# Performance work log

Measured on AMD Instinct MI355X. Metric: run time of the kernel, lower is better.

The kernel has to match this reference:

```python
import jax, jax.numpy as jnp
import numpy as np

SEQ, BS, DIM = 2048, 2, 256
G, NQ = 2, 8           # n_keys groups, n_queries total
SUB = NQ // G          # queries per group
EPS = 1e-5


def _ln(x, gamma, beta):
    m = jnp.mean(x, axis=-1, keepdims=True)
    v = jnp.mean(jnp.square(x - m), axis=-1, keepdims=True)
    return (x - m) * jax.lax.rsqrt(v + EPS) * gamma + beta


def setup_inputs() -> dict:
    key = jax.random.key(0)
    ks = jax.random.split(key, 16)
    s = 0.02
    return {
        "x":   jax.random.normal(ks[0], (SEQ, BS, DIM), jnp.float32),
        # block layernorms
        "g0": jnp.ones((DIM,), jnp.float32), "b0": jnp.zeros((DIM,), jnp.float32),
        "g1": jnp.ones((DIM,), jnp.float32), "b1": jnp.zeros((DIM,), jnp.float32),
        # attention q/k layernorm (norm_kvs=True)
        "gn": jnp.ones((DIM,), jnp.float32), "bn": jnp.zeros((DIM,), jnp.float32),
        # attention projections (torch Linear: weight [out,in])
        "wk": jax.random.normal(ks[1], (DIM * G, DIM), jnp.float32) * s,
        "bk": jnp.zeros((DIM * G,), jnp.float32),
        "wv": jax.random.normal(ks[2], (DIM * G, DIM), jnp.float32) * s,
        "bv": jnp.zeros((DIM * G,), jnp.float32),
        "wq": jax.random.normal(ks[3], (DIM * NQ, DIM), jnp.float32) * s,
        "bq": jnp.zeros((DIM * NQ,), jnp.float32),
        "wo": jax.random.normal(ks[4], (DIM, DIM * NQ), jnp.float32) * s,
        "bo": jnp.zeros((DIM,), jnp.float32),
        # FFN: BayesLora(dim,2dim) -> relu -> BayesLora(2dim,dim), eval == plain linear
        "w1": jax.random.normal(ks[5], (2 * DIM, DIM), jnp.float32) * s,
        "bf1": jnp.zeros((2 * DIM,), jnp.float32),
        "w2": jax.random.normal(ks[6], (DIM, 2 * DIM), jnp.float32) * s,
        "bf2": jnp.zeros((DIM,), jnp.float32),
    }


def reference(x, g0, b0, g1, b1, gn, bn, wk, bk, wv, bv, wq, bq, wo, bo, w1, bf1, w2, bf2):
    seq, bs, dim = x.shape
    # --- attention (pre-norm) ---
    h = _ln(x, g0, b0)                                        # s b d
    K = (h @ wk.T + bk).reshape(seq, bs, G, dim)              # s b g i
    V = (h @ wv.T + bv).reshape(seq, bs, G, dim)              # s b g i
    Q = (h @ wq.T + bq).reshape(seq, bs, G, SUB, dim)         # s b g u i
    K = _ln(K, gn, bn)
    Q = _ln(Q, gn, bn)
    scores = jnp.einsum('sbgui,tbgi->bgust', Q, K) / jnp.sqrt(jnp.float32(dim))
    neg = jnp.finfo(scores.dtype).min
    causal = jnp.tril(jnp.ones((seq, seq), bool))             # s1 >= s2 allowed
    scores = jnp.where(causal, scores, neg)
    probs = jax.nn.softmax(scores, axis=-1)                   # b g u s t
    out = jnp.einsum('bgust,tbgi->sbgui', probs, V)
    out = out.reshape(seq, bs, G * SUB * dim)                 # s b (g u i)
    x = x + (out @ wo.T + bo)
    # --- FFN (pre-norm) ---
    h2 = _ln(x, g1, b1)
    f = jax.nn.relu(h2 @ w1.T + bf1) @ w2.T + bf2
    return x + f
```

## Files before the change

kernel.cpp:

```cpp
#include <hip/hip_runtime.h>
#include <hip/hip_bf16.h>

#define SEQ  2048
#define BSZ  2
#define DIM  256
#define NG   2
#define NQH  8
#define SUBQ 4
#define ROWS (SEQ*BSZ)
#define NQKV 3072
#define QROW 6144

typedef unsigned int uint32;
typedef unsigned short ushort;
typedef __attribute__((ext_vector_type(8))) short short8;
typedef __attribute__((ext_vector_type(4))) float f32x4;

__device__ __forceinline__ float bflo(uint32 u){
  union { uint32 i; float f; } c; c.i = u << 16; return c.f;
}
__device__ __forceinline__ float bfhi(uint32 u){
  union { uint32 i; float f; } c; c.i = u & 0xffff0000u; return c.f;
}
__device__ __forceinline__ uint32 pack2(float a, float b){
  __hip_bfloat16 ha = __float2bfloat16(a);
  __hip_bfloat16 hb = __float2bfloat16(b);
  unsigned short ua, ub;
  __builtin_memcpy(&ua, &ha, 2);
  __builtin_memcpy(&ub, &hb, 2);
  return (uint32)ua | ((uint32)ub << 16);
}
__device__ __forceinline__ ushort bf16bits(float v){
  __hip_bfloat16 h = __float2bfloat16(v);
  ushort u; __builtin_memcpy(&u, &h, 2); return u;
}

__device__ __forceinline__ void dma16(const void* g, void* l) {
  __builtin_amdgcn_global_load_lds(
      (const __attribute__((address_space(1))) uint32*)g,
      (__attribute__((address_space(3))) uint32*)l, 16, 0, 0);
}

__global__ __launch_bounds__(256) void wcvt6(
    const float* __restrict__ wk, const float* __restrict__ wv,
    const float* __restrict__ wq, const float* __restrict__ wo,
    const float* __restrict__ w1, const float* __restrict__ w2,
    const float* __restrict__ bk, const float* __restrict__ bv,
    const float* __restrict__ bq,
    __hip_bfloat16* __restrict__ out, float* __restrict__ bc)
{
  int e4 = blockIdx.x * 256 + threadIdx.x;
  if (e4 < 393216) {
    const float* src; int loc;
    if      (e4 <  32768) { src = wk; loc = e4; }
    else if (e4 <  65536) { src = wv; loc = e4 -  32768; }
    else if (e4 < 196608) { src = wq; loc = e4 -  65536; }
    else if (e4 < 327680) { src = wo; loc = e4 - 196608; }
    else if (e4 < 360448) { src = w1; loc = e4 - 327680; }
    else                  { src = w2; loc = e4 - 360448; }
    float4 v = *(const float4*)(src + 4 * (size_t)loc);
    uint2 st; st.x = pack2(v.x, v.y); st.y = pack2(v.z, v.w);
    *(uint2*)(out + 4 * (size_t)e4) = st;
  } else {
    int u = e4 - 393216;
    const float* src; int loc;
    if      (u < 128) { src = bk; loc = u; }
    else if (u < 256) { src = bv; loc = u - 128; }
    else              { src = bq; loc = u - 256; }
    *(float4*)(bc + 4 * (size_t)u) = *(const float4*)(src + 4 * (size_t)loc);
  }
}

__global__ __launch_bounds__(256) void ln_rows_w(
    const float* __restrict__ in,
    const float* __restrict__ gamma,
    const float* __restrict__ beta,
    __hip_bfloat16* __restrict__ out)
{
  int wave = threadIdx.x >> 6, lane = threadIdx.x & 63;
  int row = blockIdx.x * 4 + wave;
  size_t base = (size_t)row * DIM + lane * 4;
  float4 v = *(const float4*)(in + base);
  float s  = v.x + v.y + v.z + v.w;
  float s2 = v.x*v.x + v.y*v.y + v.z*v.z + v.w*v.w;
  #pragma unroll
  for (int o = 1; o < 64; o <<= 1) {
    s  += __shfl_xor(s, o);
    s2 += __shfl_xor(s2, o);
  }
  float m = s * (1.0f / DIM);
  float rb = rsqrtf(s2 * (1.0f / DIM) - m * m + 1e-5f);
  float4 gm = *(const float4*)(gamma + lane * 4);
  float4 bt = *(const float4*)(beta + lane * 4);
  uint2 st;
  st.x = pack2((v.x - m) * rb * gm.x + bt.x, (v.y - m) * rb * gm.y + bt.y);
  st.y = pack2((v.z - m) * rb * gm.z + bt.z, (v.w - m) * rb * gm.w + bt.w);
  *(uint2*)(out + base) = st;
}

__global__ __launch_bounds__(256) void ln_qkv_w(
    __hip_bfloat16* __restrict__ QKV,
    const float* __restrict__ gamma,
    const float* __restrict__ beta)
{
  int wave = threadIdx.x >> 6, lane = threadIdx.x & 63;
  int idx = blockIdx.x * 4 + wave;
  size_t base;
  if (idx < ROWS * NG) {
    base = (size_t)(idx >> 1) * NQKV + (idx & 1) * DIM;
  } else {
    int j = idx - ROWS * NG;
    base = (size_t)(j >> 3) * NQKV + 2 * NG * DIM + (j & 7) * DIM;
  }
  __hip_bfloat16* p = QKV + base + lane * 4;
  uint2 u = *(const uint2*)p;
  float v0 = bflo(u.x), v1 = bfhi(u.x), v2 = bflo(u.y), v3 = bfhi(u.y);
  float s  = v0 + v1 + v2 + v3;
  float s2 = v0*v0 + v1*v1 + v2*v2 + v3*v3;
  #pragma unroll
  for (int o = 1; o < 64; o <<= 1) {
    s  += __shfl_xor(s, o);
    s2 += __shfl_xor(s2, o);
  }
  float m = s * (1.0f / DIM);
  float rb = rsqrtf(s2 * (1.0f / DIM) - m * m + 1e-5f);
  float4 gm = *(const float4*)(gamma + lane * 4);
  float4 bt = *(const float4*)(beta + lane * 4);
  uint2 st;
  st.x = pack2((v0 - m) * rb * gm.x + bt.x, (v1 - m) * rb * gm.y + bt.y);
  st.y = pack2((v2 - m) * rb * gm.z + bt.z, (v3 - m) * rb * gm.w + bt.w);
  *(uint2*)p = st;
}

__global__ __launch_bounds__(256) void v_transpose(
    const __hip_bfloat16* __restrict__ QKV, __hip_bfloat16* __restrict__ VT)
{
  __shared__ ushort T[64][72];
  int t0 = blockIdx.x * 64, d0 = blockIdx.y * 64, bg = blockIdx.z;
  int b = bg >> 1, g = bg & 1;
  int tid = threadIdx.x;
  int tr = tid >> 2, c4 = (tid & 3) * 16;
  const ushort* src = (const ushort*)QKV + ((size_t)(t0 + tr) * BSZ + b) * NQKV
                    + NG * DIM + g * DIM + d0 + c4;
  uint4 a0 = *(const uint4*)src;
  uint4 a1 = *(const uint4*)(src + 8);
  *(uint4*)&T[tr][c4]     = a0;
  *(uint4*)&T[tr][c4 + 8] = a1;
  __syncthreads();
  ushort tmp[16];
  #pragma unroll
  for (int i = 0; i < 16; ++i) tmp[i] = T[c4 + i][tr];
  ushort* dst = (ushort*)VT + ((size_t)bg * DIM + d0 + tr) * SEQ + t0 + c4;
  *(uint4*)dst       = *(uint4*)&tmp[0];
  *(uint4*)(dst + 8) = *(uint4*)&tmp[8];
}

template<int GN, int RELU, int OUTMODE>
__global__ __launch_bounds__(256) void gemm_mfma(
    const __hip_bfloat16* __restrict__ A,
    const __hip_bfloat16* __restrict__ W,
    const float* __restrict__ bias,
    const float* __restrict__ resid,
    void* __restrict__ outp,
    int M, int N, int K)
{
  constexpr int WCH = GN / 16;
  constexpr int MC  = (GN == 128) ? 4 : 2;
  __shared__ __align__(16) ushort AS[2][4096];
  __shared__ __align__(16) ushort WS[2][WCH * 512];

  const int tid = threadIdx.x;
  const int wave = tid >> 6, lane = tid & 63;
  const int col = lane & 15, quad = lane >> 4;
  const int wm = (GN == 128) ? (wave >> 1) : wave;
  const int wn = (GN == 128) ? (wave & 1) : 0;
  const int bn0 = blockIdx.x * GN;
  const int bm0 = blockIdx.y * 128;
  const int Keff  = (OUTMODE == 2) ? (K / gridDim.z) : K;
  const int kbase = (OUTMODE == 2) ? blockIdx.z * Keff : 0;
  const int kiters = Keff >> 5;

  f32x4 acc[MC][4];
  #pragma unroll
  for (int mc = 0; mc < MC; ++mc)
    #pragma unroll
    for (int nc = 0; nc < 4; ++nc)
      acc[mc][nc] = (f32x4){0.f, 0.f, 0.f, 0.f};

  auto stage = [&](int it, int bufi) {
    int k0 = kbase + it * 32;
    #pragma unroll
    for (int c = 0; c < 2; ++c) {
      int ch = wave * 2 + c;
      dma16((const ushort*)A + (size_t)(bm0 + ch * 16 + col) * K + k0 + quad * 8,
            &AS[bufi][ch * 512]);
    }
    #pragma unroll
    for (int c = 0; c < WCH / 4; ++c) {
      int ch = wave * (WCH / 4) + c;
      dma16((const ushort*)W + (size_t)(bn0 + ch * 16 + col) * K + k0 + quad * 8,
            &WS[bufi][ch * 512]);
    }
  };

  stage(0, 0);
  for (int it = 0; it < kiters; ++it) {
    int cur = it & 1;
    __syncthreads();
    if (it + 1 < kiters) stage(it + 1, 1 - cur);
    short8 af[MC], bf_[4];
    #pragma unroll
    for (int mc = 0; mc < MC; ++mc)
      af[mc] = *(const short8*)&AS[cur][(wm * MC + mc) * 512 + lane * 8];
    #pragma unroll
    for (int nc = 0; nc < 4; ++nc)
      bf_[nc] = *(const short8*)&WS[cur][(wn * 4 + nc) * 512 + lane * 8];
    #pragma unroll
    for (int mc = 0; mc < MC; ++mc)
      #pragma unroll
      for (int nc = 0; nc < 4; ++nc)
        acc[mc][nc] = __builtin_amdgcn_mfma_f32_16x16x32_bf16(af[mc], bf_[nc], acc[mc][nc], 0, 0, 0);
  }

  #pragma unroll
  for (int nc = 0; nc < 4; ++nc) {
    int n = bn0 + wn * 64 + nc * 16 + col;
    float bv = 0.f;
    if (OUTMODE != 2) bv = bias[n];
    #pragma unroll
    for (int mc = 0; mc < MC; ++mc) {
      #pragma unroll
      for (int reg = 0; reg < 4; ++reg) {
        int m = bm0 + wm * (MC * 16) + mc * 16 + quad * 4 + reg;
        float v = acc[mc][nc][reg] + bv;
        if (OUTMODE != 2 && resid) v += resid[(size_t)m * N + n];
        if (RELU) v = fmaxf(v, 0.f);
        if (OUTMODE == 0)
          ((__hip_bfloat16*)outp)[(size_t)m * N + n] = __float2bfloat16(v);
        else if (OUTMODE == 1)
          ((float*)outp)[(size_t)m * N + n] = v;
        else
          ((float*)outp)[(size_t)blockIdx.z * M * N + (size_t)m * N + n] = v;
      }
    }
  }
}

__global__ __launch_bounds__(256) void combine2(
    const float* __restrict__ P, const float* __restrict__ bias,
    const float* __restrict__ resid, float* __restrict__ out, int MN)
{
  int i4 = (blockIdx.x * 256 + threadIdx.x) * 4;
  float4 a = *(const float4*)(P + i4);
  float4 b = *(const float4*)(P + MN + i4);
  float4 r = *(const float4*)(resid + i4);
  float4 bb = *(const float4*)(bias + (i4 & (DIM - 1)));
  float4 o;
  o.x = a.x + b.x + r.x + bb.x;
  o.y = a.y + b.y + r.y + bb.y;
  o.z = a.z + b.z + r.z + bb.z;
  o.w = a.w + b.w + r.w + bb.w;
  *(float4*)(out + i4) = o;
}

__global__ __launch_bounds__(256) void combine_ln2(
    const float* __restrict__ P, const float* __restrict__ bias,
    const float* __restrict__ resid, float* __restrict__ X2,
    const float* __restrict__ gamma, const float* __restrict__ beta,
    __hip_bfloat16* __restrict__ H2)
{
  const int MN = ROWS * DIM;
  int wave = threadIdx.x >> 6, lane = threadIdx.x & 63;
  int row = blockIdx.x * 4 + wave;
  size_t i = (size_t)row * DIM + lane * 4;
  float4 a = *(const float4*)(P + i);
  float4 b = *(const float4*)(P + MN + i);
  float4 r = *(const float4*)(resid + i);
  float4 bb = *(const float4*)(bias + lane * 4);
  float4 v;
  v.x = a.x + b.x + r.x + bb.x;
  v.y = a.y + b.y + r.y + bb.y;
  v.z = a.z + b.z + r.z + bb.z;
  v.w = a.w + b.w + r.w + bb.w;
  *(float4*)(X2 + i) = v;
  float s  = v.x + v.y + v.z + v.w;
  float s2 = v.x*v.x + v.y*v.y + v.z*v.z + v.w*v.w;
  #pragma unroll
  for (int o = 1; o < 64; o <<= 1) {
    s  += __shfl_xor(s, o);
    s2 += __shfl_xor(s2, o);
  }
  float m = s * (1.0f / DIM);
  float rb = rsqrtf(s2 * (1.0f / DIM) - m * m + 1e-5f);
  float4 gm = *(const float4*)(gamma + lane * 4);
  float4 bt = *(const float4*)(beta + lane * 4);
  uint2 st;
  st.x = pack2((v.x - m) * rb * gm.x + bt.x, (v.y - m) * rb * gm.y + bt.y);
  st.y = pack2((v.z - m) * rb * gm.z + bt.z, (v.w - m) * rb * gm.w + bt.w);
  *(uint2*)(H2 + i) = st;
}

__global__ __launch_bounds__(256, 2) void attn_mfma(
    const __hip_bfloat16* __restrict__ QKV,
    const __hip_bfloat16* __restrict__ VTp,
    __hip_bfloat16* __restrict__ Ob,
    __hip_bfloat16* __restrict__ Op1,
    float* __restrict__ Lp)
{
  __shared__ __align__(16) ushort KS[2][8192];
  __shared__ __align__(16) ushort VS[2][8192];
  __shared__ __align__(16) ushort Pw[4][1280];

  const int tid  = threadIdx.x;
  const int wave = tid >> 6, lane = tid & 63;
  const int col  = lane & 15, quad = lane >> 4;
  const int head = blockIdx.x & 15;
  const int w    = blockIdx.x >> 4;
  int qb, z, split, nit, k0;
  if (w < 24) { qb = 15 - (w >> 1); z = w & 1; split = 1; nit = 2 * qb + 2; k0 = z * nit; }
  else        { qb = 27 - w;        z = 0;     split = 0; nit = 4 * qb + 4; k0 = 0; }

  const int b = head >> 3, hq = head & 7, g = hq >> 2;
  const int bg = b * NG + g;
  const int qw0 = qb * 128 + wave * 32;

  short8 qf[2][8];
  #pragma unroll
  for (int mc = 0; mc < 2; ++mc) {
    int s = qw0 + mc * 16 + col;
    const ushort* qp = (const ushort*)QKV + (size_t)s * QROW + b * NQKV
                     + 2 * NG * DIM + hq * DIM + quad * 8;
    #pragma unroll
    for (int ks = 0; ks < 8; ++ks)
      qf[mc][ks] = *(const short8*)(qp + ks * 32);
  }

  short8 onesf;
  #pragma unroll
  for (int i = 0; i < 8; ++i) onesf[i] = (short)0x3F80;

  f32x4 o[2][16];
  #pragma unroll
  for (int mc = 0; mc < 2; ++mc)
    #pragma unroll
    for (int dc = 0; dc < 16; ++dc)
      o[mc][dc] = (f32x4){0.f, 0.f, 0.f, 0.f};
  float l_s[2][4] = {{0.f}};

  auto stage = [&](int i, int bufi) {
    int kt = k0 + i;
    #pragma unroll
    for (int cc = 0; cc < 4; ++cc) {
      int nk = wave * 4 + cc;
      int tc = nk >> 3, ksl = nk & 7;
      const ushort* gk = (const ushort*)QKV
          + ((size_t)(kt * 32 + tc * 16 + col) * BSZ + b) * NQKV
          + g * DIM + ksl * 32 + quad * 8;
      dma16(gk, &KS[bufi][nk * 512]);
      const ushort* gv = (const ushort*)VTp
          + ((size_t)bg * DIM + nk * 16 + col) * SEQ + kt * 32 + quad * 8;
      dma16(gv, &VS[bufi][nk * 512]);
    }
  };

  stage(0, 0);
  for (int i = 0; i < nit; ++i) {
    int cur = i & 1;
    __syncthreads();
    if (i + 1 < nit) stage(i + 1, 1 - cur);
    int kt = k0 + i;
    if (kt * 32 > qw0 + 31) continue;

    f32x4 sf[2][2];
    #pragma unroll
    for (int mc = 0; mc < 2; ++mc)
      #pragma unroll
      for (int tc = 0; tc < 2; ++tc)
        sf[mc][tc] = (f32x4){0.f, 0.f, 0.f, 0.f};
    #pragma unroll
    for (int ks = 0; ks < 8; ++ks) {
      short8 kb0 = *(const short8*)&KS[cur][ks * 512 + lane * 8];
      short8 kb1 = *(const short8*)&KS[cur][(8 + ks) * 512 + lane * 8];
      sf[0][0] = __builtin_amdgcn_mfma_f32_16x16x32_bf16(qf[0][ks], kb0, sf[0][0], 0, 0, 0);
      sf[0][1] = __builtin_amdgcn_mfma_f32_16x16x32_bf16(qf[0][ks], kb1, sf[0][1], 0, 0, 0);
      sf[1][0] = __builtin_amdgcn_mfma_f32_16x16x32_bf16(qf[1][ks], kb0, sf[1][0], 0, 0, 0);
      sf[1][1] = __builtin_amdgcn_mfma_f32_16x16x32_bf16(qf[1][ks], kb1, sf[1][1], 0, 0, 0);
    }

    const bool dm = (kt * 32 + 31) > qw0;
    #pragma unroll
    for (int mc = 0; mc < 2; ++mc)
      #pragma unroll
      for (int tc = 0; tc < 2; ++tc)
        #pragma unroll
        for (int reg = 0; reg < 4; ++reg) {
          float p = __expf(sf[mc][tc][reg] * 0.0625f);
          if (dm) {
            int tg = kt * 32 + tc * 16 + col;
            int sg = qw0 + mc * 16 + quad * 4 + reg;
            if (tg > sg) p = 0.f;
          }
          Pw[wave][(mc * 16 + quad * 4 + reg) * 40 + tc * 16 + col] = bf16bits(p);
        }

    short8 pa0 = *(const short8*)&Pw[wave][col * 40 + quad * 8];
    short8 pa1 = *(const short8*)&Pw[wave][(16 + col) * 40 + quad * 8];

    f32x4 zz = (f32x4){0.f, 0.f, 0.f, 0.f};
    f32x4 ps0 = __builtin_amdgcn_mfma_f32_16x16x32_bf16(pa0, onesf, zz, 0, 0, 0);
    f32x4 ps1 = __builtin_amdgcn_mfma_f32_16x16x32_bf16(pa1, onesf, zz, 0, 0, 0);
    #pragma unroll
    for (int r = 0; r < 4; ++r) { l_s[0][r] += ps0[r]; l_s[1][r] += ps1[r]; }

    #pragma unroll
    for (int dc = 0; dc < 16; ++dc) {
      short8 vb = *(const short8*)&VS[cur][dc * 512 + lane * 8];
      o[0][dc] = __builtin_amdgcn_mfma_f32_16x16x32_bf16(pa0, vb, o[0][dc], 0, 0, 0);
      o[1][dc] = __builtin_amdgcn_mfma_f32_16x16x32_bf16(pa1, vb, o[1][dc], 0, 0, 0);
    }
  }

  if (!split) {
    #pragma unroll
    for (int mc = 0; mc < 2; ++mc)
      #pragma unroll
      for (int reg = 0; reg < 4; ++reg) {
        float inv = 1.0f / l_s[mc][reg];
        int s = qw0 + mc * 16 + quad * 4 + reg;
        __hip_bfloat16* op = Ob + (size_t)s * (BSZ * NQH * DIM) + b * (NQH * DIM) + hq * DIM;
        #pragma unroll
        for (int dc = 0; dc < 16; ++dc)
          op[dc * 16 + col] = __float2bfloat16(o[mc][dc][reg] * inv);
      }
  } else {
    #pragma unroll
    for (int mc = 0; mc < 2; ++mc)
      #pragma unroll
      for (int reg = 0; reg < 4; ++reg) {
        int s = qw0 + mc * 16 + quad * 4 + reg;
        int row = s - 512;
        __hip_bfloat16* op = (z == 0)
            ? Ob  + (size_t)s   * (BSZ * NQH * DIM) + b * (NQH * DIM) + hq * DIM
            : Op1 + (size_t)row * (BSZ * NQH * DIM) + b * (NQH * DIM) + hq * DIM;
        #pragma unroll
        for (int dc = 0; dc < 16; ++dc)
          op[dc * 16 + col] = __float2bfloat16(o[mc][dc][reg]);
        if (col == 0) Lp[(z * 1536 + row) * 16 + head] = l_s[mc][reg];
      }
  }
}

__global__ __launch_bounds__(256) void attn_norm(
    __hip_bfloat16* __restrict__ Ob, const __hip_bfloat16* __restrict__ Op1,
    const float* __restrict__ Lp)
{
  int i4 = (blockIdx.x * 256 + threadIdx.x) * 4;
  int row = i4 >> 12;
  int off = i4 & 4095;
  int head = off >> 8;
  float inv = 1.0f / (Lp[row * 16 + head] + Lp[(1536 + row) * 16 + head]);
  ushort* a = (ushort*)Ob + (size_t)(row + 512) * 4096 + off;
  const ushort* c = (const ushort*)Op1 + (size_t)row * 4096 + off;
  uint2 ua = *(const uint2*)a;
  uint2 uc = *(const uint2*)c;
  uint2 st;
  st.x = pack2((bflo(ua.x) + bflo(uc.x)) * inv, (bfhi(ua.x) + bfhi(uc.x)) * inv);
  st.y = pack2((bflo(ua.y) + bflo(uc.y)) * inv, (bfhi(ua.y) + bfhi(uc.y)) * inv);
  *(uint2*)a = st;
}

extern "C" void kernel_launch(void* const* d_in, const int* in_sizes, int n_in,
                              void* d_out, int out_size, void* d_ws, size_t ws_size,
                              hipStream_t stream)
{
  const float* x   = (const float*)d_in[0];
  const float* g0  = (const float*)d_in[1];
  const float* b0  = (const float*)d_in[2];
  const float* g1  = (const float*)d_in[3];
  const float* b1  = (const float*)d_in[4];
  const float* gn  = (const float*)d_in[5];
  const float* bn  = (const float*)d_in[6];
  const float* wk  = (const float*)d_in[7];
  const float* bk  = (const float*)d_in[8];
  const float* wv  = (const float*)d_in[9];
  const float* bv  = (const float*)d_in[10];
  const float* wq  = (const float*)d_in[11];
  const float* bq  = (const float*)d_in[12];
  const float* wo  = (const float*)d_in[13];
  const float* bo  = (const float*)d_in[14];
  const float* w1  = (const float*)d_in[15];
  const float* bf1 = (const float*)d_in[16];
  const float* w2  = (const float*)d_in[17];
  const float* bf2 = (const float*)d_in[18];

  char* ws = (char*)d_ws;
  const size_t MB = 1024 * 1024;
  __hip_bfloat16* QKV = (__hip_bfloat16*)(ws);
  float*          Pwo = (float*)         (ws);
  float*          X2  = (float*)         (ws + 8  * MB);
  __hip_bfloat16* H2  = (__hip_bfloat16*)(ws + 12 * MB);
  __hip_bfloat16* F1  = (__hip_bfloat16*)(ws + 14 * MB);
  float*          Pw2 = (float*)         (ws + 18 * MB);
  __hip_bfloat16* VT  = (__hip_bfloat16*)(ws + 24 * MB);
  __hip_bfloat16* H   = (__hip_bfloat16*)(ws + 26 * MB);
  __hip_bfloat16* AO  = (__hip_bfloat16*)(ws + 28 * MB);
  __hip_bfloat16* Op1 = (__hip_bfloat16*)(ws + 44 * MB);
  __hip_bfloat16* WB  = (__hip_bfloat16*)(ws + 57 * MB);
  float*          BC  = (float*)         (ws + 60 * MB);
  float*          Lp  = (float*)         (ws + 60 * MB + 16 * 1024);

  __hip_bfloat16* woB = WB + 786432;
  __hip_bfloat16* w1B = WB + 1310720;
  __hip_bfloat16* w2B = WB + 1441792;

  wcvt6<<<1539, 256, 0, stream>>>(wk, wv, wq, wo, w1, w2, bk, bv, bq, WB, BC);
  ln_rows_w<<<ROWS / 4, 256, 0, stream>>>(x, g0, b0, H);
  gemm_mfma<128,0,0><<<dim3(NQKV/128, ROWS/128), 256, 0, stream>>>(H, WB, BC, nullptr, QKV, ROWS, NQKV, DIM);
  ln_qkv_w<<<(ROWS * NG + ROWS * NQH) / 4, 256, 0, stream>>>(QKV, gn, bn);
  v_transpose<<<dim3(SEQ/64, DIM/64, BSZ*NG), 256, 0, stream>>>(QKV, VT);
  attn_mfma<<<448, 256, 0, stream>>>(QKV, VT, AO, Op1, Lp);
  attn_norm<<<6144, 256, 0, stream>>>(AO, Op1, Lp);
  gemm_mfma<64,0,2><<<dim3(DIM/64, ROWS/128, 2), 256, 0, stream>>>(AO, woB, nullptr, nullptr, Pwo, ROWS, DIM, NQH*DIM);
  combine_ln2<<<ROWS / 4, 256, 0, stream>>>(Pwo, bo, x, X2, g1, b1, H2);
  gemm_mfma<64,1,0><<<dim3((2*DIM)/64, ROWS/128), 256, 0, stream>>>(H2, w1B, bf1, nullptr, F1, ROWS, 2*DIM, DIM);
  gemm_mfma<64,0,2><<<dim3(DIM/64, ROWS/128, 2), 256, 0, stream>>>(F1, w2B, nullptr, nullptr, Pw2, ROWS, DIM, 2*DIM);
  combine2<<<ROWS*DIM/1024, 256, 0, stream>>>(Pw2, bf2, X2, (float*)d_out, ROWS*DIM);
}
```

Baseline: 290.8 us.

## Pre-swizzle weights, K and V into MFMA fragment-contiguous layout for DMA

Weights are converted to bf16 directly in the 16x32 fragment-tiled order the GEMM's LDS DMA consumes, so each wave's weight load reads one contiguous 1 KB chunk instead of 16 strided rows. K is copied by a new kernel into per-tile contiguous fragments, and the V transpose now writes the same fragment layout, so the attention kernel streams both with contiguous addresses. The goal is better coalescing in the GEMM and attention inner loops. It costs one extra kernel launch and an extra copy of K, and the workspace offsets are reshuffled.

```diff
diff --git a/kernel.cpp b/kernel.cpp
--- a/kernel.cpp
+++ b/kernel.cpp
@@ -49,25 +49,43 @@
     const float* __restrict__ bq,
     __hip_bfloat16* __restrict__ out, float* __restrict__ bc)
 {
-  int e4 = blockIdx.x * 256 + threadIdx.x;
-  if (e4 < 393216) {
+  int u = blockIdx.x * 256 + threadIdx.x;
+  if (u < 196608) {
+    int lane = u & 63, col = lane & 15, quad = lane >> 4;
+    const float* srcrow;
+    if (u < 98304) {
+      int n16 = u >> 9, kc = (u >> 6) & 7;
+      int n = n16 * 16 + col;
+      const float* m = (n < 512) ? (wk + (size_t)n * 256)
+                     : (n < 1024) ? (wv + (size_t)(n - 512) * 256)
+                                  : (wq + (size_t)(n - 1024) * 256);
+      srcrow = m + kc * 32 + quad * 8;
+    } else if (u < 163840) {
+      int local = u - 98304;
+      int n16 = local >> 12, kc = (local >> 6) & 63;
+      srcrow = wo + (size_t)(n16 * 16 + col) * 2048 + kc * 32 + quad * 8;
+    } else if (u < 180224) {
+      int local = u - 163840;
+      int n16 = local >> 9, kc = (local >> 6) & 7;
+      srcrow = w1 + (size_t)(n16 * 16 + col) * 256 + kc * 32 + quad * 8;
+    } else {
+      int local = u - 180224;
+      int n16 = local >> 10, kc = (local >> 6) & 15;
+      srcrow = w2 + (size_t)(n16 * 16 + col) * 512 + kc * 32 + quad * 8;
+    }
+    float4 a = *(const float4*)srcrow;
+    float4 b = *(const float4*)(srcrow + 4);
+    uint4 st;
+    st.x = pack2(a.x, a.y); st.y = pack2(a.z, a.w);
+    st.z = pack2(b.x, b.y); st.w = pack2(b.z, b.w);
+    *(uint4*)((ushort*)out + (size_t)u * 8) = st;
+  } else {
+    int bu = u - 196608;
     const float* src; int loc;
-    if      (e4 <  32768) { src = wk; loc = e4; }
-    else if (e4 <  65536) { src = wv; loc = e4 -  32768; }
-    else if (e4 < 196608) { src = wq; loc = e4 -  65536; }
-    else if (e4 < 327680) { src = wo; loc = e4 - 196608; }
-    else if (e4 < 360448) { src = w1; loc = e4 - 327680; }
-    else                  { src = w2; loc = e4 - 360448; }
-    float4 v = *(const float4*)(src + 4 * (size_t)loc);
-    uint2 st; st.x = pack2(v.x, v.y); st.y = pack2(v.z, v.w);
-    *(uint2*)(out + 4 * (size_t)e4) = st;
-  } else {
-    int u = e4 - 393216;
-    const float* src; int loc;
-    if      (u < 128) { src = bk; loc = u; }
-    else if (u < 256) { src = bv; loc = u - 128; }
-    else              { src = bq; loc = u - 256; }
-    *(float4*)(bc + 4 * (size_t)u) = *(const float4*)(src + 4 * (size_t)loc);
+    if      (bu < 128) { src = bk; loc = bu; }
+    else if (bu < 256) { src = bv; loc = bu - 128; }
+    else               { src = bq; loc = bu - 256; }
+    *(float4*)(bc + 4 * (size_t)bu) = *(const float4*)(src + 4 * (size_t)loc);
   }
 }
 
@@ -132,8 +150,23 @@
   *(uint2*)p = st;
 }
 
-__global__ __launch_bounds__(256) void v_transpose(
-    const __hip_bfloat16* __restrict__ QKV, __hip_bfloat16* __restrict__ VT)
+__global__ __launch_bounds__(256) void kf_swizzle(
+    const __hip_bfloat16* __restrict__ QKV, __hip_bfloat16* __restrict__ Kf)
+{
+  int wave = threadIdx.x >> 6, lane = threadIdx.x & 63;
+  int col = lane & 15, quad = lane >> 4;
+  int cid = blockIdx.x * 4 + wave;
+  int nk = cid & 15, kt = (cid >> 4) & 63, bg = cid >> 10;
+  int b = bg >> 1, g = bg & 1;
+  int tc = nk >> 3, ks = nk & 7;
+  const ushort* src = (const ushort*)QKV
+      + ((size_t)(kt * 32 + tc * 16 + col) * BSZ + b) * NQKV + g * DIM + ks * 32 + quad * 8;
+  uint4 v = *(const uint4*)src;
+  *(uint4*)((ushort*)Kf + (size_t)cid * 512 + lane * 8) = v;
+}
+
+__global__ __launch_bounds__(256) void v_swizzle(
+    const __hip_bfloat16* __restrict__ QKV, __hip_bfloat16* __restrict__ Vf)
 {
   __shared__ ushort T[64][72];
   int t0 = blockIdx.x * 64, d0 = blockIdx.y * 64, bg = blockIdx.z;
@@ -147,12 +180,18 @@
   *(uint4*)&T[tr][c4]     = a0;
   *(uint4*)&T[tr][c4 + 8] = a1;
   __syncthreads();
-  ushort tmp[16];
-  #pragma unroll
-  for (int i = 0; i < 16; ++i) tmp[i] = T[c4 + i][tr];
-  ushort* dst = (ushort*)VT + ((size_t)bg * DIM + d0 + tr) * SEQ + t0 + c4;
-  *(uint4*)dst       = *(uint4*)&tmp[0];
-  *(uint4*)(dst + 8) = *(uint4*)&tmp[8];
+  #pragma unroll
+  for (int k2 = 0; k2 < 2; ++k2) {
+    int u = tid * 2 + k2;
+    int tt = u >> 8, di = (u >> 6) & 3, qd = (u >> 4) & 3, cl = u & 15;
+    ushort tmp[8];
+    #pragma unroll
+    for (int e = 0; e < 8; ++e) tmp[e] = T[tt * 32 + qd * 8 + e][di * 16 + cl];
+    int kt = (t0 >> 5) + tt;
+    int dc = (d0 >> 4) + di;
+    *(uint4*)((ushort*)Vf + (((size_t)(bg * 64 + kt) * 16 + dc) << 9) + (qd * 16 + cl) * 8)
+        = *(uint4*)tmp;
+  }
 }
 
 template<int GN, int RELU, int OUTMODE>
@@ -198,7 +237,7 @@
     #pragma unroll
     for (int c = 0; c < WCH / 4; ++c) {
       int ch = wave * (WCH / 4) + c;
-      dma16((const ushort*)W + (size_t)(bn0 + ch * 16 + col) * K + k0 + quad * 8,
+      dma16((const ushort*)W + (((size_t)((bn0 >> 4) + ch) * (K >> 5) + (k0 >> 5)) << 9) + lane * 8,
             &WS[bufi][ch * 512]);
     }
   };
@@ -302,7 +341,8 @@
 
 __global__ __launch_bounds__(256, 2) void attn_mfma(
     const __hip_bfloat16* __restrict__ QKV,
-    const __hip_bfloat16* __restrict__ VTp,
+    const __hip_bfloat16* __restrict__ Kf,
+    const __hip_bfloat16* __restrict__ Vf,
     __hip_bfloat16* __restrict__ Ob,
     __hip_bfloat16* __restrict__ Op1,
     float* __restrict__ Lp)
@@ -349,17 +389,13 @@
 
   auto stage = [&](int i, int bufi) {
     int kt = k0 + i;
+    const ushort* kb = (const ushort*)Kf + (((size_t)bg * 64 + kt) << 13);
+    const ushort* vb = (const ushort*)Vf + (((size_t)bg * 64 + kt) << 13);
     #pragma unroll
     for (int cc = 0; cc < 4; ++cc) {
       int nk = wave * 4 + cc;
-      int tc = nk >> 3, ksl = nk & 7;
-      const ushort* gk = (const ushort*)QKV
-          + ((size_t)(kt * 32 + tc * 16 + col) * BSZ + b) * NQKV
-          + g * DIM + ksl * 32 + quad * 8;
-      dma16(gk, &KS[bufi][nk * 512]);
-      const ushort* gv = (const ushort*)VTp
-          + ((size_t)bg * DIM + nk * 16 + col) * SEQ + kt * 32 + quad * 8;
-      dma16(gv, &VS[bufi][nk * 512]);
+      dma16(kb + (nk << 9) + lane * 8, &KS[bufi][nk * 512]);
+      dma16(vb + (nk << 9) + lane * 8, &VS[bufi][nk * 512]);
     }
   };
 
@@ -501,24 +537,26 @@
   __hip_bfloat16* H2  = (__hip_bfloat16*)(ws + 12 * MB);
   __hip_bfloat16* F1  = (__hip_bfloat16*)(ws + 14 * MB);
   float*          Pw2 = (float*)         (ws + 18 * MB);
-  __hip_bfloat16* VT  = (__hip_bfloat16*)(ws + 24 * MB);
-  __hip_bfloat16* H   = (__hip_bfloat16*)(ws + 26 * MB);
-  __hip_bfloat16* AO  = (__hip_bfloat16*)(ws + 28 * MB);
-  __hip_bfloat16* Op1 = (__hip_bfloat16*)(ws + 44 * MB);
-  __hip_bfloat16* WB  = (__hip_bfloat16*)(ws + 57 * MB);
-  float*          BC  = (float*)         (ws + 60 * MB);
-  float*          Lp  = (float*)         (ws + 60 * MB + 16 * 1024);
+  __hip_bfloat16* H   = (__hip_bfloat16*)(ws + 24 * MB);
+  __hip_bfloat16* Kf  = (__hip_bfloat16*)(ws + 24 * MB);
+  __hip_bfloat16* Vf  = (__hip_bfloat16*)(ws + 28 * MB);
+  __hip_bfloat16* AO  = (__hip_bfloat16*)(ws + 32 * MB);
+  __hip_bfloat16* Op1 = (__hip_bfloat16*)(ws + 48 * MB);
+  float*          BC  = (float*)         (ws + 60 * MB + 768 * 1024);
+  float*          Lp  = (float*)         (ws + 60 * MB + 800 * 1024);
+  __hip_bfloat16* WB  = (__hip_bfloat16*)(ws + 61 * MB);
 
   __hip_bfloat16* woB = WB + 786432;
   __hip_bfloat16* w1B = WB + 1310720;
   __hip_bfloat16* w2B = WB + 1441792;
 
-  wcvt6<<<1539, 256, 0, stream>>>(wk, wv, wq, wo, w1, w2, bk, bv, bq, WB, BC);
+  wcvt6<<<771, 256, 0, stream>>>(wk, wv, wq, wo, w1, w2, bk, bv, bq, WB, BC);
   ln_rows_w<<<ROWS / 4, 256, 0, stream>>>(x, g0, b0, H);
   gemm_mfma<128,0,0><<<dim3(NQKV/128, ROWS/128), 256, 0, stream>>>(H, WB, BC, nullptr, QKV, ROWS, NQKV, DIM);
   ln_qkv_w<<<(ROWS * NG + ROWS * NQH) / 4, 256, 0, stream>>>(QKV, gn, bn);
-  v_transpose<<<dim3(SEQ/64, DIM/64, BSZ*NG), 256, 0, stream>>>(QKV, VT);
-  attn_mfma<<<448, 256, 0, stream>>>(QKV, VT, AO, Op1, Lp);
+  kf_swizzle<<<1024, 256, 0, stream>>>(QKV, Kf);
+  v_swizzle<<<dim3(SEQ/64, DIM/64, BSZ*NG), 256, 0, stream>>>(QKV, Vf);
+  attn_mfma<<<448, 256, 0, stream>>>(QKV, Kf, Vf, AO, Op1, Lp);
   attn_norm<<<6144, 256, 0, stream>>>(AO, Op1, Lp);
   gemm_mfma<64,0,2><<<dim3(DIM/64, ROWS/128, 2), 256, 0, stream>>>(AO, woB, nullptr, nullptr, Pwo, ROWS, DIM, NQH*DIM);
   combine_ln2<<<ROWS / 4, 256, 0, stream>>>(Pwo, bo, x, X2, g1, b1, H2);
```

After: 259.1 us. 1.12x faster.
